# Kernel tuning notes

Hardware: AMD Instinct MI355X
Metric: run time of the kernel (lower is better)

## Reference

```python
import jax, jax.numpy as jnp
import numpy as np

NUM_STEPS = 20
BETA = 0.9
THR = 1.0
B, D, H, O = 8192, 784, 128, 10


def setup_inputs() -> dict:
    key = jax.random.key(0)
    k1, k2, k3, k4, k5 = jax.random.split(key, 5)
    x = jax.random.uniform(k1, (B, D), jnp.float32)  # rates in [0,1]
    lim1 = 1.0 / np.sqrt(D)
    lim2 = 1.0 / np.sqrt(H)
    fc1_w = jax.random.uniform(k2, (H, D), jnp.float32, -lim1, lim1)
    fc1_b = jax.random.uniform(k3, (H,), jnp.float32, -lim1, lim1)
    fc2_w = jax.random.uniform(k4, (O, H), jnp.float32, -lim2, lim2)
    fc2_b = jax.random.uniform(k5, (O,), jnp.float32, -lim2, lim2)
    return {"x": x, "fc1_w": fc1_w, "fc1_b": fc1_b, "fc2_w": fc2_w, "fc2_b": fc2_b}


def heaviside(u):
    return (u > 0).astype(u.dtype)


def lif_step(mem, cur):
    # snntorch Leaky, reset_mechanism='subtract':
    #   reset computed from incoming mem, then mem = beta*mem + cur - reset*thr
    reset = heaviside(mem - THR)
    mem = BETA * mem + cur - reset * THR
    spk = heaviside(mem - THR)
    return spk, mem


def reference(x, fc1_w, fc1_b, fc2_w, fc2_b):
    batch = x.shape[0]
    # spikegen.rate: per-step Bernoulli with probability x (fixed key -> deterministic)
    skey = jax.random.key(42)
    x_spike = jax.random.bernoulli(skey, x, (NUM_STEPS, batch, x.shape[1])).astype(x.dtype)

    mem1 = jnp.zeros((batch, fc1_w.shape[0]), x.dtype)
    mem2 = jnp.zeros((batch, fc2_w.shape[0]), x.dtype)

    def step(carry, x_t):
        m1, m2 = carry
        cur1 = x_t @ fc1_w.T + fc1_b          # [B,128]
        spk1, m1 = lif_step(m1, cur1)
        cur2 = spk1 @ fc2_w.T + fc2_b         # [B,10]
        spk2, m2 = lif_step(m2, cur2)
        return (m1, m2), spk2

    _, spk2_stack = jax.lax.scan(step, (mem1, mem2), x_spike)  # [T,B,10]
    return spk2_stack.sum(axis=0) / NUM_STEPS
```

## Files before the change

### kernel.cpp

```cpp
#include <hip/hip_runtime.h>
#include <cstdint>


#define T_STEPS 20
#define B_SZ   8192
#define D_SZ   784
#define H_SZ   128
#define O_SZ   10
#define CUR1_BYTES  83886080u
#define MASKS_BYTES 655360u
#define WPLANE_OFF  (CUR1_BYTES + MASKS_BYTES)

typedef __attribute__((ext_vector_type(8))) short short8;
typedef __attribute__((ext_vector_type(4))) float f32x4;
typedef unsigned short ushort_t;

__device__ __forceinline__ uint32_t rotl32(uint32_t x, uint32_t d) {
  return (x << d) | (x >> (32u - d));
}

__device__ __forceinline__ void threefry_0_42(uint32_t c0, uint32_t c1,
                                              uint32_t& o0, uint32_t& o1) {
  const uint32_t ks0 = 0u;
  const uint32_t ks1 = 42u;
  const uint32_t ks2 = 0u ^ 42u ^ 0x1BD11BDAu;
  uint32_t x0 = c0 + ks0;
  uint32_t x1 = c1 + ks1;
#define TF_R(rot) { x0 += x1; x1 = rotl32(x1, rot); x1 ^= x0; }
  TF_R(13u) TF_R(15u) TF_R(26u) TF_R(6u)
  x0 += ks1; x1 += ks2 + 1u;
  TF_R(17u) TF_R(29u) TF_R(16u) TF_R(24u)
  x0 += ks2; x1 += ks0 + 2u;
  TF_R(13u) TF_R(15u) TF_R(26u) TF_R(6u)
  x0 += ks0; x1 += ks1 + 3u;
  TF_R(17u) TF_R(29u) TF_R(16u) TF_R(24u)
  x0 += ks1; x1 += ks2 + 4u;
  TF_R(13u) TF_R(15u) TF_R(26u) TF_R(6u)
  x0 += ks2; x1 += ks0 + 5u;
#undef TF_R
  o0 = x0; o1 = x1;
}

__device__ __forceinline__ float tf_uniform(uint32_t bits) {
  return __uint_as_float((bits >> 9) | 0x3f800000u) - 1.0f;
}

__device__ __forceinline__ uint32_t rne_bf16_bits(float f) {
  uint32_t u = __float_as_uint(f);
  return (u + 0x7fffu + ((u >> 16) & 1u)) & 0xffff0000u;
}

__global__ __launch_bounds__(256) void split_w1(
    const float* __restrict__ w1, ushort_t* __restrict__ wp) {
  const int h = blockIdx.x;
  for (int k = threadIdx.x; k < 800; k += 256) {
    float w = (k < D_SZ) ? w1[h * D_SZ + k] : 0.0f;
    uint32_t hb = rne_bf16_bits(w);
    float hi = __uint_as_float(hb);
    float r1 = w - hi;
    uint32_t mb = rne_bf16_bits(r1);
    float mid = __uint_as_float(mb);
    float lo = r1 - mid;
    uint32_t lb = __float_as_uint(lo);
    wp[0 * 102400 + h * 800 + k] = (ushort_t)(hb >> 16);
    wp[1 * 102400 + h * 800 + k] = (ushort_t)(mb >> 16);
    wp[2 * 102400 + h * 800 + k] = (ushort_t)(lb >> 16);
  }
}

__global__ __launch_bounds__(256) void spike_gemm1_mfma(
    const float* __restrict__ x, const ushort_t* __restrict__ wp,
    const float* __restrict__ b1, float* __restrict__ cur1) {
  __shared__ __align__(16) ushort_t sS[128 * 40];
  __shared__ __align__(16) ushort_t sW[3][128 * 40];

  const int tid  = threadIdx.x;
  const int row0 = blockIdx.x << 7;
  const int wave = tid >> 6, lane = tid & 63;
  const int wr0  = (wave >> 1) << 6;
  const int wc0  = (wave & 1) << 6;
  const int lm   = lane & 15, quad = lane >> 4;

  f32x4 acc[4][4];
#pragma unroll
  for (int m = 0; m < 4; ++m)
#pragma unroll
    for (int nn = 0; nn < 4; ++nn) acc[m][nn] = (f32x4){0.f, 0.f, 0.f, 0.f};

  const int srow  = tid & 127;
  const int shalf = tid >> 7;
  const uint32_t nbase = (uint32_t)(row0 + srow) * 784u;
  const float* xrow = x + (size_t)((uint32_t)(row0 + srow) & 8191u) * D_SZ;

  for (int ko = 0; ko < 25; ++ko) {
    const int k0 = ko << 5;
    __syncthreads();
#pragma unroll
    for (int i = 0; i < 6; ++i) {
      int u = tid + (i << 8);
      int p = u >> 9;
      int v = u & 511;
      int h = v >> 2, kp = v & 3;
      const short8 g = *(const short8*)&wp[p * 102400 + h * 800 + k0 + kp * 8];
      *(short8*)&sW[p][h * 40 + kp * 8] = g;
    }
    {
      const int kbase = k0 + shalf * 16;
      short8 s0 = (short8)0, s1 = (short8)0;
      if (kbase < D_SZ) {
#pragma unroll
        for (int q = 0; q < 4; ++q) {
          float4 xv = *(const float4*)&xrow[kbase + q * 4];
          float pr[4] = {xv.x, xv.y, xv.z, xv.w};
#pragma unroll
          for (int jj = 0; jj < 4; ++jj) {
            int j = q * 4 + jj;
            uint32_t n = nbase + (uint32_t)(kbase + j);
            uint32_t o0, o1;
            threefry_0_42(0u, n, o0, o1);
            short sv = (tf_uniform(o0 ^ o1) < pr[jj]) ? (short)0x3F80 : (short)0;
            if (j < 8) s0[j] = sv; else s1[j - 8] = sv;
          }
        }
      }
      *(short8*)&sS[srow * 40 + shalf * 16]     = s0;
      *(short8*)&sS[srow * 40 + shalf * 16 + 8] = s1;
    }
    __syncthreads();
    short8 a[4];
#pragma unroll
    for (int m = 0; m < 4; ++m)
      a[m] = *(const short8*)&sS[(wr0 + m * 16 + lm) * 40 + quad * 8];
#pragma unroll
    for (int p = 0; p < 3; ++p) {
#pragma unroll
      for (int nn = 0; nn < 4; ++nn) {
        short8 bfr = *(const short8*)&sW[p][(wc0 + nn * 16 + lm) * 40 + quad * 8];
#pragma unroll
        for (int m = 0; m < 4; ++m)
          acc[m][nn] = __builtin_amdgcn_mfma_f32_16x16x32_bf16(
              a[m], bfr, acc[m][nn], 0, 0, 0);
      }
    }
  }

#pragma unroll
  for (int nn = 0; nn < 4; ++nn) {
    int col = wc0 + nn * 16 + lm;
    float bias = b1[col];
#pragma unroll
    for (int m = 0; m < 4; ++m) {
#pragma unroll
      for (int r = 0; r < 4; ++r) {
        int grow = row0 + wr0 + m * 16 + quad * 4 + r;
        cur1[(size_t)grow * H_SZ + col] = acc[m][nn][r] + bias;
      }
    }
  }
}

__global__ __launch_bounds__(256) void lif1_spikes(
    const float* __restrict__ cur1, uint32_t* __restrict__ masks) {
#pragma clang fp contract(off)
  const int g   = blockIdx.x * 256 + threadIdx.x;
  const int row = g >> 2;
  const int p   = g & 3;

  float mem1[32];
#pragma unroll
  for (int i = 0; i < 32; ++i) mem1[i] = 0.0f;

  const float4* base = (const float4*)cur1;

  for (int t = 0; t < T_STEPS; ++t) {
    size_t rb = ((size_t)t * B_SZ + (size_t)row) * (H_SZ / 4) + p;
    float4 c[8];
#pragma unroll
    for (int j = 0; j < 8; ++j) c[j] = base[rb + (size_t)j * 4];

    uint32_t spkbits = 0u;
#pragma unroll
    for (int j = 0; j < 8; ++j) {
      float cv[4] = {c[j].x, c[j].y, c[j].z, c[j].w};
#pragma unroll
      for (int q = 0; q < 4; ++q) {
        int i = j * 4 + q;
        float m = mem1[i];
        float reset = (m > 1.0f) ? 1.0f : 0.0f;
        m = 0.9f * m;
        m = m + cv[q];
        m = m - reset;
        mem1[i] = m;
        spkbits |= (m > 1.0f) ? (1u << i) : 0u;
      }
    }
    uint32_t myword = 0u;
#pragma unroll
    for (int w = 0; w < 4; ++w) {
      uint32_t part = (((spkbits >> (8 * w)) & 0xFu) << (4 * p)) |
                      (((spkbits >> (8 * w + 4)) & 0xFu) << (16 + 4 * p));
      part |= __shfl_xor(part, 1);
      part |= __shfl_xor(part, 2);
      if (w == p) myword = part;
    }
    masks[(size_t)t * (B_SZ * 4) + (size_t)g] = myword;
  }
}

__global__ __launch_bounds__(320) void lif2_seq(
    const float* __restrict__ w2, const float* __restrict__ b2,
    const uint32_t* __restrict__ masks, float* __restrict__ out) {
#pragma clang fp contract(off)
  __shared__ __align__(16) float sW2[O_SZ][H_SZ];
  const int tid = threadIdx.x;
  for (int i = tid; i < O_SZ * H_SZ; i += 320)
    sW2[i >> 7][i & 127] = w2[i];
  __syncthreads();

  const int wave = tid >> 6;
  const int lane = tid & 63;
  const int row  = ((blockIdx.x >> 1) << 6) + lane;
  const int o    = (blockIdx.x & 1) * 5 + wave;
  const float bias = b2[o];

  float mem2 = 0.0f;
  int cnt = 0;
  const uint4* mbase = (const uint4*)masks;

  for (int t = 0; t < T_STEPS; ++t) {
    uint4 m = mbase[(size_t)t * B_SZ + row];
    uint32_t mw[4] = {m.x, m.y, m.z, m.w};
    float acc = 0.0f;
#pragma unroll
    for (int w = 0; w < 4; ++w) {
#pragma unroll
      for (int hc = 0; hc < 8; ++hc) {
        float4 wv = *(const float4*)&sW2[o][w * 32 + hc * 4];
        float vv[4] = {wv.x, wv.y, wv.z, wv.w};
#pragma unroll
        for (int bb = 0; bb < 4; ++bb) {
          float val = ((mw[w] >> (hc * 4 + bb)) & 1u) ? vv[bb] : 0.0f;
          acc = acc + val;
        }
      }
    }
    float c2 = acc + bias;
    float reset = (mem2 > 1.0f) ? 1.0f : 0.0f;
    mem2 = 0.9f * mem2;
    mem2 = mem2 + c2;
    mem2 = mem2 - reset;
    cnt += (mem2 > 1.0f) ? 1 : 0;
  }
  out[row * O_SZ + o] = (float)cnt / 20.0f;
}

extern "C" void kernel_launch(void* const* d_in, const int* in_sizes, int n_in,
                              void* d_out, int out_size, void* d_ws, size_t ws_size,
                              hipStream_t stream) {
  const float* x   = (const float*)d_in[0];
  const float* w1  = (const float*)d_in[1];
  const float* b1  = (const float*)d_in[2];
  const float* w2  = (const float*)d_in[3];
  const float* b2  = (const float*)d_in[4];
  float* out  = (float*)d_out;
  float* cur1 = (float*)d_ws;
  uint32_t* masks = (uint32_t*)((char*)d_ws + CUR1_BYTES);
  ushort_t* wp    = (ushort_t*)((char*)d_ws + WPLANE_OFF);

  split_w1<<<dim3(128), dim3(256), 0, stream>>>(w1, wp);
  spike_gemm1_mfma<<<dim3(1280), dim3(256), 0, stream>>>(x, wp, b1, cur1);
  lif1_spikes<<<dim3(128), dim3(256), 0, stream>>>(cur1, masks);
  lif2_seq<<<dim3(256), dim3(320), 0, stream>>>(w2, b2, masks, out);
}
```

Before: 483.1 us.

## Split spike generation into bit-packed kernel and stream GEMM operands from global

Moves the Threefry Bernoulli spike generation out of the GEMM into its own kernel, which writes 32-bit spike masks per 32 inputs. The GEMM then expands those bits into bf16 A fragments in registers and reads the weight planes straight from global memory, dropping LDS staging and both barriers. The aim is to stop RNG work from serialising the MFMA pipeline. The LIF1 kernel also gets four times as many threads, each handling 8 neurons, for more parallelism. The cost is an extra kernel launch, a small intermediate mask buffer, and uncoalesced, uncached global weight loads in the GEMM.

```diff
diff --git a/kernel.cpp b/kernel.cpp
--- a/kernel.cpp
+++ b/kernel.cpp
@@ -8,8 +8,9 @@
 #define H_SZ   128
 #define O_SZ   10
 #define CUR1_BYTES  83886080u
-#define MASKS_BYTES 655360u
-#define WPLANE_OFF  (CUR1_BYTES + MASKS_BYTES)
+#define MASKS_OFF   83886080u
+#define WP_OFF      84541440u
+#define M32_OFF     85155840u
 
 typedef __attribute__((ext_vector_type(8))) short short8;
 typedef __attribute__((ext_vector_type(4))) float f32x4;
@@ -68,18 +69,52 @@
   }
 }
 
-__global__ __launch_bounds__(256) void spike_gemm1_mfma(
-    const float* __restrict__ x, const ushort_t* __restrict__ wp,
+__global__ __launch_bounds__(256) void spikegen_bits(
+    const float* __restrict__ x, uint32_t* __restrict__ m32) {
+  const int g = blockIdx.x * 256 + threadIdx.x;
+  const int b = g / 25;
+  const int w = g - b * 25;
+  const int d0 = w << 5;
+
+  float pr[32];
+  {
+    const float* xr = x + (size_t)b * D_SZ + d0;
+    const int nv = (w == 24) ? 4 : 8;
+#pragma unroll
+    for (int q = 0; q < 8; ++q) {
+      float4 v;
+      if (q < nv) v = *(const float4*)&xr[q * 4];
+      else        v = (float4){0.f, 0.f, 0.f, 0.f};
+      pr[q * 4 + 0] = v.x; pr[q * 4 + 1] = v.y;
+      pr[q * 4 + 2] = v.z; pr[q * 4 + 3] = v.w;
+    }
+  }
+
+  const uint32_t bw = (uint32_t)b * 784u + (uint32_t)d0;
+#pragma unroll 1
+  for (int t = 0; t < T_STEPS; ++t) {
+    const uint32_t nb = (uint32_t)t * 6422528u + bw;
+    uint32_t word = 0u;
+#pragma unroll
+    for (int j = 0; j < 32; ++j) {
+      uint32_t o0, o1;
+      threefry_0_42(0u, nb + (uint32_t)j, o0, o1);
+      word |= (tf_uniform(o0 ^ o1) < pr[j]) ? (1u << j) : 0u;
+    }
+    m32[(size_t)(t * B_SZ + b) * 25 + w] = word;
+  }
+}
+
+__global__ __launch_bounds__(256) void gemm1_mfma(
+    const ushort_t* __restrict__ wp, const uint32_t* __restrict__ m32,
     const float* __restrict__ b1, float* __restrict__ cur1) {
-  __shared__ __align__(16) ushort_t sS[128 * 40];
-  __shared__ __align__(16) ushort_t sW[3][128 * 40];
-
   const int tid  = threadIdx.x;
   const int row0 = blockIdx.x << 7;
   const int wave = tid >> 6, lane = tid & 63;
   const int wr0  = (wave >> 1) << 6;
   const int wc0  = (wave & 1) << 6;
   const int lm   = lane & 15, quad = lane >> 4;
+  const int qsh  = quad << 3;
 
   f32x4 acc[4][4];
 #pragma unroll
@@ -87,59 +122,31 @@
 #pragma unroll
     for (int nn = 0; nn < 4; ++nn) acc[m][nn] = (f32x4){0.f, 0.f, 0.f, 0.f};
 
-  const int srow  = tid & 127;
-  const int shalf = tid >> 7;
-  const uint32_t nbase = (uint32_t)(row0 + srow) * 784u;
-  const float* xrow = x + (size_t)((uint32_t)(row0 + srow) & 8191u) * D_SZ;
+  const uint32_t* mrow = m32 + (size_t)(row0 + wr0 + lm) * 25;
+  const ushort_t* wbase = wp + (size_t)(wc0 + lm) * 800 + qsh;
 
   for (int ko = 0; ko < 25; ++ko) {
-    const int k0 = ko << 5;
-    __syncthreads();
-#pragma unroll
-    for (int i = 0; i < 6; ++i) {
-      int u = tid + (i << 8);
-      int p = u >> 9;
-      int v = u & 511;
-      int h = v >> 2, kp = v & 3;
-      const short8 g = *(const short8*)&wp[p * 102400 + h * 800 + k0 + kp * 8];
-      *(short8*)&sW[p][h * 40 + kp * 8] = g;
-    }
-    {
-      const int kbase = k0 + shalf * 16;
-      short8 s0 = (short8)0, s1 = (short8)0;
-      if (kbase < D_SZ) {
-#pragma unroll
-        for (int q = 0; q < 4; ++q) {
-          float4 xv = *(const float4*)&xrow[kbase + q * 4];
-          float pr[4] = {xv.x, xv.y, xv.z, xv.w};
-#pragma unroll
-          for (int jj = 0; jj < 4; ++jj) {
-            int j = q * 4 + jj;
-            uint32_t n = nbase + (uint32_t)(kbase + j);
-            uint32_t o0, o1;
-            threefry_0_42(0u, n, o0, o1);
-            short sv = (tf_uniform(o0 ^ o1) < pr[jj]) ? (short)0x3F80 : (short)0;
-            if (j < 8) s0[j] = sv; else s1[j - 8] = sv;
-          }
-        }
-      }
-      *(short8*)&sS[srow * 40 + shalf * 16]     = s0;
-      *(short8*)&sS[srow * 40 + shalf * 16 + 8] = s1;
-    }
-    __syncthreads();
     short8 a[4];
 #pragma unroll
-    for (int m = 0; m < 4; ++m)
-      a[m] = *(const short8*)&sS[(wr0 + m * 16 + lm) * 40 + quad * 8];
+    for (int m = 0; m < 4; ++m) {
+      uint32_t word = mrow[m * 400 + ko];
+      uint32_t byte = (word >> qsh) & 0xffu;
+      short8 av;
+#pragma unroll
+      for (int j = 0; j < 8; ++j)
+        av[j] = (short)(((byte >> j) & 1u) ? 0x3F80 : 0);
+      a[m] = av;
+    }
+    const int kof = ko << 5;
 #pragma unroll
     for (int p = 0; p < 3; ++p) {
 #pragma unroll
       for (int nn = 0; nn < 4; ++nn) {
-        short8 bfr = *(const short8*)&sW[p][(wc0 + nn * 16 + lm) * 40 + quad * 8];
+        short8 bf = *(const short8*)&wbase[p * 102400 + nn * 16 * 800 + kof];
 #pragma unroll
         for (int m = 0; m < 4; ++m)
           acc[m][nn] = __builtin_amdgcn_mfma_f32_16x16x32_bf16(
-              a[m], bfr, acc[m][nn], 0, 0, 0);
+              a[m], bf, acc[m][nn], 0, 0, 0);
       }
     }
   }
@@ -162,48 +169,38 @@
 __global__ __launch_bounds__(256) void lif1_spikes(
     const float* __restrict__ cur1, uint32_t* __restrict__ masks) {
 #pragma clang fp contract(off)
-  const int g   = blockIdx.x * 256 + threadIdx.x;
-  const int row = g >> 2;
-  const int p   = g & 3;
-
-  float mem1[32];
-#pragma unroll
-  for (int i = 0; i < 32; ++i) mem1[i] = 0.0f;
-
-  const float4* base = (const float4*)cur1;
+  const int g    = blockIdx.x * 256 + threadIdx.x;
+  const int row  = g >> 4;
+  const int s    = g & 15;
+  const int lane = threadIdx.x & 63;
+
+  float mem[8];
+#pragma unroll
+  for (int i = 0; i < 8; ++i) mem[i] = 0.0f;
 
   for (int t = 0; t < T_STEPS; ++t) {
-    size_t rb = ((size_t)t * B_SZ + (size_t)row) * (H_SZ / 4) + p;
-    float4 c[8];
-#pragma unroll
-    for (int j = 0; j < 8; ++j) c[j] = base[rb + (size_t)j * 4];
-
-    uint32_t spkbits = 0u;
-#pragma unroll
-    for (int j = 0; j < 8; ++j) {
-      float cv[4] = {c[j].x, c[j].y, c[j].z, c[j].w};
-#pragma unroll
-      for (int q = 0; q < 4; ++q) {
-        int i = j * 4 + q;
-        float m = mem1[i];
-        float reset = (m > 1.0f) ? 1.0f : 0.0f;
-        m = 0.9f * m;
-        m = m + cv[q];
-        m = m - reset;
-        mem1[i] = m;
-        spkbits |= (m > 1.0f) ? (1u << i) : 0u;
-      }
-    }
-    uint32_t myword = 0u;
-#pragma unroll
-    for (int w = 0; w < 4; ++w) {
-      uint32_t part = (((spkbits >> (8 * w)) & 0xFu) << (4 * p)) |
-                      (((spkbits >> (8 * w + 4)) & 0xFu) << (16 + 4 * p));
-      part |= __shfl_xor(part, 1);
-      part |= __shfl_xor(part, 2);
-      if (w == p) myword = part;
-    }
-    masks[(size_t)t * (B_SZ * 4) + (size_t)g] = myword;
+    const float* base = cur1 + ((size_t)t * B_SZ + row) * H_SZ + s * 8;
+    float4 c0 = *(const float4*)base;
+    float4 c1 = *(const float4*)(base + 4);
+    float cv[8] = {c0.x, c0.y, c0.z, c0.w, c1.x, c1.y, c1.z, c1.w};
+
+    uint32_t bits8 = 0u;
+#pragma unroll
+    for (int q = 0; q < 8; ++q) {
+      float m = mem[q];
+      float reset = (m > 1.0f) ? 1.0f : 0.0f;
+      m = 0.9f * m;
+      m = m + cv[q];
+      m = m - reset;
+      mem[q] = m;
+      bits8 |= (m > 1.0f) ? (1u << q) : 0u;
+    }
+    uint32_t part = bits8 << ((s & 3) * 8);
+    part |= __shfl_xor(part, 1);
+    part |= __shfl_xor(part, 2);
+    uint32_t myw = __shfl(part, (lane & ~15) + 4 * (s & 3));
+    if (s < 4)
+      masks[((size_t)t * B_SZ + row) * 4 + s] = myw;
   }
 }
 
@@ -263,12 +260,14 @@
   const float* w2  = (const float*)d_in[3];
   const float* b2  = (const float*)d_in[4];
   float* out  = (float*)d_out;
-  float* cur1 = (float*)d_ws;
-  uint32_t* masks = (uint32_t*)((char*)d_ws + CUR1_BYTES);
-  ushort_t* wp    = (ushort_t*)((char*)d_ws + WPLANE_OFF);
-
-  split_w1<<<dim3(128), dim3(256), 0, stream>>>(w1, wp);
-  spike_gemm1_mfma<<<dim3(1280), dim3(256), 0, stream>>>(x, wp, b1, cur1);
-  lif1_spikes<<<dim3(128), dim3(256), 0, stream>>>(cur1, masks);
-  lif2_seq<<<dim3(256), dim3(320), 0, stream>>>(w2, b2, masks, out);
-}
+  float*    cur1  = (float*)d_ws;
+  uint32_t* masks = (uint32_t*)((char*)d_ws + MASKS_OFF);
+  ushort_t* wp    = (ushort_t*)((char*)d_ws + WP_OFF);
+  uint32_t* m32   = (uint32_t*)((char*)d_ws + M32_OFF);
+
+  split_w1     <<<dim3(128),  dim3(256), 0, stream>>>(w1, wp);
+  spikegen_bits<<<dim3(800),  dim3(256), 0, stream>>>(x, m32);
+  gemm1_mfma   <<<dim3(1280), dim3(256), 0, stream>>>(wp, m32, b1, cur1);
+  lif1_spikes  <<<dim3(512),  dim3(256), 0, stream>>>(cur1, masks);
+  lif2_seq     <<<dim3(256),  dim3(320), 0, stream>>>(w2, b2, masks, out);
+}
```

After: 576.4 us. 19.3% more time.
